# Performance work log

Hardware: AMD Instinct MI355X
Metric: run time of the kernel (lower is better)

Reference implementation:

```python
import jax, jax.numpy as jnp
import numpy as np

EPS = 1e-08


def _d_hat(d, mask, eps=EPS):
    # d: [B,N,H,W] float, mask: [B,N,H,W] bool
    B, N, H, W = mask.shape
    flat_d = d.reshape(B * N, H * W)
    flat_m = mask.reshape(B * N, H * W)
    cnt = flat_m.sum(axis=1)  # [BN] int
    # masked median: push invalid entries to +inf, sort, pick lower-median index
    sorted_v = jnp.sort(jnp.where(flat_m, flat_d, jnp.inf), axis=1)
    idx = jnp.maximum((cnt - 1) // 2, 0)
    med = jnp.take_along_axis(sorted_v, idx[:, None], axis=1)[:, 0]
    med = jnp.where(cnt > 0, med, jnp.zeros_like(med))  # empty mask -> median 0
    cnt_f = jnp.maximum(cnt, 1).astype(d.dtype)
    # masked MAD scale (mean abs deviation over valid pixels) + eps
    abs_sum = (jnp.abs(flat_d - med[:, None]) * flat_m).sum(axis=1)
    sc = jnp.where(cnt > 0, abs_sum / cnt_f + eps, jnp.full_like(abs_sum, eps))
    d_hat = (flat_d - med[:, None]) / sc[:, None]
    return d_hat.reshape(B, N, H, W)


def _avg_pool(x, k):
    # matches F.avg_pool2d(x, k, stride=k): crop to full windows, mean per kxk block
    B, N, H, W = x.shape
    Hk, Wk = H // k, W // k
    xc = x[..., : Hk * k, : Wk * k].reshape(B, N, Hk, k, Wk, k)
    return xc.mean(axis=(3, 5))


def _grad_loss(pred, target, mask):
    total = jnp.asarray(0.0, pred.dtype)
    mf = mask.astype(pred.dtype)
    for s in range(4):
        if s == 0:
            p, t, m = pred, target, mask
        else:
            k = 2 ** s
            p = _avg_pool(pred, k)
            t = _avg_pool(target, k)
            m = _avg_pool(mf, k) > 0  # .bool() of pooled float mask
        diff = p - t
        gx = jnp.abs(diff[..., :, 1:] - diff[..., :, :-1])
        gy = jnp.abs(diff[..., 1:, :] - diff[..., :-1, :])
        mx = m[..., :, 1:] & m[..., :, :-1]
        my = m[..., 1:, :] & m[..., :-1, :]
        lx = (gx * mx).sum() / jnp.maximum(mx.sum(), 1).astype(pred.dtype)
        ly = (gy * my).sum() / jnp.maximum(my.sum(), 1).astype(pred.dtype)
        total = total + lx + ly
    return total / 4


def setup_inputs() -> dict:
    key = jax.random.key(0)
    k1, k2, k3 = jax.random.split(key, 3)
    B, N, H, W = 4, 16, 518, 518
    pred = jax.random.normal(k1, (B, N, H, W), dtype=jnp.float32)
    y = jax.random.normal(k2, (B, N, H, W), dtype=jnp.float32)
    masks_squeezed = jax.random.bernoulli(k3, 0.9, (B, N, H, W))
    return {"pred": pred, "y": y, "masks_squeezed": masks_squeezed}


def reference(pred, y, masks_squeezed):
    mask = masks_squeezed.astype(bool)
    pred_hat = _d_hat(pred, mask)
    y_hat = _d_hat(y, mask)
    rho = jnp.abs(pred_hat - y_hat) * mask  # rho[~mask] = 0
    valid = jnp.maximum(mask.sum(axis=(2, 3)).astype(pred.dtype), 1.0)
    loss_ssi = (rho.sum(axis=(2, 3)) / valid).mean()
    loss_grad = _grad_loss(pred_hat, y_hat, mask)
    return loss_ssi + 0.5 * loss_grad
```

## Files before the change

### kernel.cpp

```cpp
#include <hip/hip_runtime.h>
#include <stdint.h>

typedef unsigned int u32;
typedef unsigned long long u64;
typedef unsigned char u8;

#define NIMG 64
#define W0   518
#define H0   518
#define HW   268324
#define HW4  67081
#define BPI  32
#define NB0  33
#define N1 67081
#define N2 16641
#define CAP 32768
#define LCAP 1024

#define OFF_CNT   0ULL
#define OFF_CCNT  256ULL
#define OFF_NBL   768ULL
#define OFF_RHO   1280ULL
#define OFF_STOT  1792ULL
#define OFF_SBL   2816ULL
#define OFF_GI0   3840ULL
#define OFF_GI1   5888ULL
#define OFF_GI2   7936ULL
#define OFF_GI3   9984ULL
#define ZERO_END  12032ULL
#define OFF_MED   12032ULL
#define OFF_SCI   12544ULL
#define OFF_SELW  13056ULL
#define OFF_SWF   14080ULL
#define OFF_CAND  15360ULL
#define OFF_MU8   (OFF_CAND + 16777216ULL)
#define OFF_P1    (OFF_MU8 + 17172736ULL)
#define OFF_M1    (OFF_P1 + 17172736ULL)
#define OFF_P2    (OFF_M1 + 4293184ULL)
#define OFF_M2    (OFF_P2 + 4260096ULL)

__device__ __forceinline__ u32 f2key(float f) {
  u32 u = __float_as_uint(f);
  return (u & 0x80000000u) ? ~u : (u | 0x80000000u);
}
__device__ __forceinline__ float key2f(u32 k) {
  u32 u = (k & 0x80000000u) ? (k & 0x7fffffffu) : ~k;
  return __uint_as_float(u);
}

__device__ void blk_rankfind(u32* h, u32 target, bool enable, u32* outBin, u32* outRank)
{
  int b0 = threadIdx.x * 8;
  u32 s = 0;
  for (int j = 0; j < 8; j++) s += h[b0 + j];
  u32 x = s;
  int lane = threadIdx.x & 63;
  for (int o = 1; o < 64; o <<= 1) {
    u32 v = __shfl_up(x, o, 64);
    if (lane >= o) x += v;
  }
  __shared__ u32 wsum[4];
  int wv = threadIdx.x >> 6;
  if (lane == 63) wsum[wv] = x;
  __syncthreads();
  u32 woff = 0;
  for (int w = 0; w < wv; w++) woff += wsum[w];
  u32 cum = woff + x - s;
  for (int j = 0; j < 8; j++) {
    u32 v = h[b0 + j];
    if (enable && target >= cum && target < cum + v) { *outBin = (u32)(b0 + j); *outRank = target - cum; }
    cum += v;
  }
  __syncthreads();
}

__global__ __launch_bounds__(256) void k_sample(const float* __restrict__ p,
    const float* __restrict__ y, u32* __restrict__ selw, float* __restrict__ swf,
    u32* __restrict__ zbase)
{
  int t = blockIdx.x, img = t >> 1;
  if (t == 0) {
    for (int i = threadIdx.x; i < 3008; i += 256) zbase[i] = 0;
  }
  const float* src = ((t & 1) ? y : p) + (size_t)img * HW;
  __shared__ u32 h[2048];
  __shared__ u32 bLo, rT, bHi;
  if (threadIdx.x == 0) { bLo = 0; bHi = 2047; }
  for (int i = threadIdx.x; i < 2048; i += 256) h[i] = 0;
  __syncthreads();
  for (int j = 0; j < 16; j++) {
    int s = threadIdx.x * 16 + j;
    float v = src[s * 65 + 32];
    atomicAdd(&h[f2key(v) >> 21], 1u);
  }
  __syncthreads();
  blk_rankfind(h, 1919u, true, &bLo, &rT);
  blk_rankfind(h, 2175u, true, &bHi, &rT);
  if (threadIdx.x == 0) {
    u32 k0 = bLo << 21;
    u32 k1 = (bHi >= 2047u) ? 0xFFFFFFFFu : ((bHi + 1u) << 21);
    selw[2 * t + 0] = k0;
    selw[2 * t + 1] = k1;
    float f0 = (k0 <= 0x007FFFFFu) ? __uint_as_float(0xFF800000u) : key2f(k0);
    float f1 = (k1 >= 0xFF800000u) ? __uint_as_float(0x7F800000u) : key2f(k1);
    swf[2 * t + 0] = f0;
    swf[2 * t + 1] = f1;
  }
}

__global__ __launch_bounds__(256) void k_scan0(const float4* __restrict__ p,
    const float4* __restrict__ y, const int4* __restrict__ m,
    uchar4* __restrict__ mu4, const float* __restrict__ swf,
    float* __restrict__ cand, u32* __restrict__ ccnt, u32* __restrict__ cnt,
    double* __restrict__ Stot, u32* __restrict__ Nbl, double* __restrict__ Sbl)
{
  __shared__ float capP[LCAP], capY[LCAP];
  __shared__ u32 nP, nY, baseP, baseY;
  if (threadIdx.x == 0) { nP = 0; nY = 0; }
  __syncthreads();
  int img = blockIdx.x / BPI, blk = blockIdx.x % BPI;
  float f0P = swf[img * 4 + 0], f1P = swf[img * 4 + 1];
  float f0Y = swf[img * 4 + 2], f1Y = swf[img * 4 + 3];
  const float4* pb = p + (size_t)img * HW4;
  const float4* yb = y + (size_t)img * HW4;
  const int4* mb = m + (size_t)img * HW4;
  uchar4* mo = mu4 + (size_t)img * HW4;
  int lc = 0, nBp = 0, nBy = 0;
  float sTp = 0.f, sBp = 0.f, sTy = 0.f, sBy = 0.f;

#define PEL(mm, vp, vy) if (mm) { lc++; \
      sTp += vp; \
      if (vp < f0P) { nBp++; sBp += vp; } \
      else if (vp < f1P) { u32 ix = atomicAdd(&nP, 1u); if (ix < LCAP) capP[ix] = vp; } \
      sTy += vy; \
      if (vy < f0Y) { nBy++; sBy += vy; } \
      else if (vy < f1Y) { u32 ix = atomicAdd(&nY, 1u); if (ix < LCAP) capY[ix] = vy; } }
#define PGRP(idx) { \
      float4 pv = pb[idx]; float4 yv = yb[idx]; int4 mv = mb[idx]; \
      uchar4 mw; mw.x = mv.x ? 1 : 0; mw.y = mv.y ? 1 : 0; mw.z = mv.z ? 1 : 0; mw.w = mv.w ? 1 : 0; \
      mo[idx] = mw; \
      PEL(mw.x, pv.x, yv.x) PEL(mw.y, pv.y, yv.y) PEL(mw.z, pv.z, yv.z) PEL(mw.w, pv.w, yv.w) }

  const int S = BPI * 256;
  int i = blk * 256 + threadIdx.x;
  for (; i + S < HW4; i += 2 * S) {
    float4 pa = pb[i], pc = pb[i + S];
    float4 ya = yb[i], yc = yb[i + S];
    int4 ma = mb[i], mc = mb[i + S];
    uchar4 wa, wc;
    wa.x = ma.x ? 1 : 0; wa.y = ma.y ? 1 : 0; wa.z = ma.z ? 1 : 0; wa.w = ma.w ? 1 : 0;
    wc.x = mc.x ? 1 : 0; wc.y = mc.y ? 1 : 0; wc.z = mc.z ? 1 : 0; wc.w = mc.w ? 1 : 0;
    mo[i] = wa; mo[i + S] = wc;
    PEL(wa.x, pa.x, ya.x) PEL(wa.y, pa.y, ya.y) PEL(wa.z, pa.z, ya.z) PEL(wa.w, pa.w, ya.w)
    PEL(wc.x, pc.x, yc.x) PEL(wc.y, pc.y, yc.y) PEL(wc.z, pc.z, yc.z) PEL(wc.w, pc.w, yc.w)
  }
  if (i < HW4) PGRP(i)
#undef PGRP
#undef PEL

  __syncthreads();
  if (threadIdx.x == 0) {
    u32 np = nP, ny = nY;
    u32 addP = (np > (u32)LCAP) ? (u32)(CAP + 1) : np;
    u32 addY = (ny > (u32)LCAP) ? (u32)(CAP + 1) : ny;
    baseP = atomicAdd(&ccnt[img * 2 + 0], addP);
    baseY = atomicAdd(&ccnt[img * 2 + 1], addY);
  }
  __syncthreads();
  {
    u32 np = min(nP, (u32)LCAP), ny = min(nY, (u32)LCAP);
    float* cp = cand + (size_t)(img * 2 + 0) * CAP;
    float* cy = cand + (size_t)(img * 2 + 1) * CAP;
    for (u32 k = threadIdx.x; k < np; k += 256) { u32 g = baseP + k; if (g < CAP) cp[g] = capP[k]; }
    for (u32 k = threadIdx.x; k < ny; k += 256) { u32 g = baseY + k; if (g < CAP) cy[g] = capY[k]; }
  }
  double v0 = (double)sTp, v1 = (double)sBp, v2 = (double)sTy, v3 = (double)sBy;
  double v4 = (double)lc, v5 = (double)nBp, v6 = (double)nBy;
  for (int o = 32; o; o >>= 1) {
    v0 += __shfl_down(v0, o, 64); v1 += __shfl_down(v1, o, 64);
    v2 += __shfl_down(v2, o, 64); v3 += __shfl_down(v3, o, 64);
    v4 += __shfl_down(v4, o, 64); v5 += __shfl_down(v5, o, 64);
    v6 += __shfl_down(v6, o, 64);
  }
  __shared__ double sh[7][4];
  int lane = threadIdx.x & 63, wv = threadIdx.x >> 6;
  if (lane == 0) { sh[0][wv]=v0; sh[1][wv]=v1; sh[2][wv]=v2; sh[3][wv]=v3; sh[4][wv]=v4; sh[5][wv]=v5; sh[6][wv]=v6; }
  __syncthreads();
  if (threadIdx.x == 0) {
    double a[7];
    for (int k = 0; k < 7; k++) a[k] = sh[k][0] + sh[k][1] + sh[k][2] + sh[k][3];
    atomicAdd(&Stot[img * 2 + 0], a[0]);
    atomicAdd(&Sbl [img * 2 + 0], a[1]);
    atomicAdd(&Stot[img * 2 + 1], a[2]);
    atomicAdd(&Sbl [img * 2 + 1], a[3]);
    atomicAdd(&cnt[img], (u32)a[4]);
    atomicAdd(&Nbl[img * 2 + 0], (u32)a[5]);
    atomicAdd(&Nbl[img * 2 + 1], (u32)a[6]);
  }
}

__global__ __launch_bounds__(256) void k_med2(const float* __restrict__ cand,
    const u32* __restrict__ ccnt, const u32* __restrict__ cnt,
    const u32* __restrict__ Nbl, const double* __restrict__ Stot,
    const double* __restrict__ Sbl, const u32* __restrict__ selw,
    const float* __restrict__ pf, const float* __restrict__ yf,
    const u8* __restrict__ mu8, float* __restrict__ med, float* __restrict__ sci)
{
  int t = blockIdx.x, img = t >> 1;
  u32 c = cnt[img];
  if (c == 0) {
    if (threadIdx.x == 0) { med[t] = 0.f; sci[t] = 1e8f; }
    return;
  }
  u32 ntot = ccnt[t];
  u32 target0 = (c - 1) >> 1;
  u32 nb = Nbl[t];
  bool valid = (ntot <= (u32)CAP) && (target0 >= nb) && ((target0 - nb) < ntot);
  __shared__ u32 h[2048];
  __shared__ u32 sBin, sRank;
  if (threadIdx.x == 0) { sBin = 0; sRank = 0; }
  int lane = threadIdx.x & 63, wv = threadIdx.x >> 6;
  __shared__ double sh2[2][4];

  if (valid) {
    u32 n = ntot;
    const float* cd = cand + (size_t)t * CAP;
    u32 curLo = selw[2 * t + 0];
    u64 curR = (u64)selw[2 * t + 1] - (u64)curLo;
    u32 tgt = target0 - nb;
    for (int pass = 0; pass < 3; pass++) {
      int s = 0;
      while (((curR - 1) >> s) >= 2048) s++;
      for (int i = threadIdx.x; i < 2048; i += 256) h[i] = 0;
      __syncthreads();
      for (u32 j = threadIdx.x; j < n; j += 256) {
        u32 k = f2key(cd[j]);
        if (k >= curLo && (u64)(k - curLo) < curR)
          atomicAdd(&h[(k - curLo) >> s], 1u);
      }
      __syncthreads();
      blk_rankfind(h, tgt, true, &sBin, &sRank);
      curLo = curLo + (sBin << s);
      curR = (u64)1 << s;
      tgt = sRank;
      if (s == 0) break;
    }
    float mv = key2f(curLo);
    u32 nlt2 = 0; float slt2 = 0.f;
    for (u32 j = threadIdx.x; j < n; j += 256) {
      float v = cd[j];
      if (v < mv) { nlt2++; slt2 += v; }
    }
    double v0 = (double)nlt2, v1 = (double)slt2;
    for (int o = 32; o; o >>= 1) { v0 += __shfl_down(v0, o, 64); v1 += __shfl_down(v1, o, 64); }
    if (lane == 0) { sh2[0][wv] = v0; sh2[1][wv] = v1; }
    __syncthreads();
    if (threadIdx.x == 0) {
      double nl = (double)nb + sh2[0][0] + sh2[0][1] + sh2[0][2] + sh2[0][3];
      double sl = Sbl[t] + sh2[1][0] + sh2[1][1] + sh2[1][2] + sh2[1][3];
      double md = (double)mv;
      double mad = Stot[t] + 2.0 * md * nl - 2.0 * sl - md * (double)c;
      double sc = mad / (double)c + 1e-8;
      med[t] = mv; sci[t] = (float)(1.0 / sc);
    }
  } else {
    const float* src = ((t & 1) ? yf : pf) + (size_t)img * HW;
    const u8* mk = mu8 + (size_t)img * HW;
    u32 curLo = 0; u64 curR = (u64)1 << 32; u32 tgt = target0;
    for (int pass = 0; pass < 4; pass++) {
      int s = 0;
      while (((curR - 1) >> s) >= 2048) s++;
      for (int i = threadIdx.x; i < 2048; i += 256) h[i] = 0;
      __syncthreads();
      for (u32 j = threadIdx.x; j < (u32)HW; j += 256) {
        if (mk[j]) {
          u32 k = f2key(src[j]);
          if (k >= curLo && (u64)(k - curLo) < curR)
            atomicAdd(&h[(k - curLo) >> s], 1u);
        }
      }
      __syncthreads();
      blk_rankfind(h, tgt, true, &sBin, &sRank);
      curLo = curLo + (sBin << s);
      curR = (u64)1 << s;
      tgt = sRank;
      if (s == 0) break;
    }
    float mv = key2f(curLo);
    double nl = 0.0, sl = 0.0;
    for (u32 j = threadIdx.x; j < (u32)HW; j += 256) {
      if (mk[j]) {
        float v = src[j];
        if (v < mv) { nl += 1.0; sl += (double)v; }
      }
    }
    for (int o = 32; o; o >>= 1) { nl += __shfl_down(nl, o, 64); sl += __shfl_down(sl, o, 64); }
    if (lane == 0) { sh2[0][wv] = nl; sh2[1][wv] = sl; }
    __syncthreads();
    if (threadIdx.x == 0) {
      double nlT = sh2[0][0] + sh2[0][1] + sh2[0][2] + sh2[0][3];
      double slT = sh2[1][0] + sh2[1][1] + sh2[1][2] + sh2[1][3];
      double md = (double)mv;
      double mad = Stot[t] + 2.0 * md * nlT - 2.0 * slT - md * (double)c;
      double sc = mad / (double)c + 1e-8;
      med[t] = mv; sci[t] = (float)(1.0 / sc);
    }
  }
}

__global__ __launch_bounds__(320) void k_fuse0(const float* __restrict__ p,
    const float* __restrict__ y, const u8* __restrict__ mu,
    const float* __restrict__ medv, const float* __restrict__ sciv,
    float* __restrict__ P1, u8* __restrict__ M1,
    double* __restrict__ rho, double* __restrict__ gI)
{
  int img = blockIdx.x / NB0, band = blockIdx.x % NB0;
  float mp = medv[img * 2 + 0], my = medv[img * 2 + 1];
  float ap = sciv[img * 2 + 0], ay = sciv[img * 2 + 1];
  const float* pb = p + (size_t)img * HW;
  const float* yb = y + (size_t)img * HW;
  const u8*   mb = mu + (size_t)img * HW;
  int ra = band * 16;
  int rb = min(ra + 16, H0);
  int rend = (rb < H0) ? rb + 1 : H0;
  int oc = threadIdx.x;
  bool act = oc < 259;
  int cc = act ? 2 * oc : 516;
  bool vn = act && (2 * oc + 2 < W0);
  int lane = threadIdx.x & 63;
  bool edge = (lane == 63);
  float gx = 0.f, gy = 0.f, rr = 0.f;
  int cx = 0, cy = 0;
  float pd0 = 0.f, pd1 = 0.f; u8 pm0 = 0, pm1 = 0;
  float2 pv0, yv0, pv1, yv1;
  uchar2 mv0, mv1;
  {
    size_t a0 = (size_t)ra * W0 + cc;
    pv0 = *(const float2*)(pb + a0); yv0 = *(const float2*)(yb + a0); mv0 = *(const uchar2*)(mb + a0);
    if (ra + 1 < rend) {
      size_t a1 = a0 + W0;
      pv1 = *(const float2*)(pb + a1); yv1 = *(const float2*)(yb + a1); mv1 = *(const uchar2*)(mb + a1);
    } else { pv1 = pv0; yv1 = yv0; mv1 = mv0; }
  }
  for (int r = ra; r < rend; ++r) {
    float2 pv2 = pv1, yv2 = yv1; uchar2 mv2 = mv1;
    if (r + 2 < rend) {
      size_t a2 = (size_t)(r + 2) * W0 + cc;
      pv2 = *(const float2*)(pb + a2); yv2 = *(const float2*)(yb + a2); mv2 = *(const uchar2*)(mb + a2);
    }
    bool core = r < rb;
    float d0 = (pv0.x - mp) * ap - (yv0.x - my) * ay;
    float d1 = (pv0.y - mp) * ap - (yv0.y - my) * ay;
    u8 m0 = mv0.x, m1 = mv0.y;
    float dn = __shfl_down(d0, 1, 64);
    int mn = __shfl_down((int)m0, 1, 64);
    if (vn && edge) {
      size_t a = (size_t)r * W0 + (size_t)cc + 2;
      float pnb = pb[a], ynb = yb[a];
      dn = (pnb - mp) * ap - (ynb - my) * ay;
      mn = mb[a];
    }
    if (act) {
      float f0 = (float)m0, f1 = (float)m1;
      if (core) {
        gx += f0 * f1 * fabsf(d1 - d0); cx += (int)(m0 & m1);
        if (vn) { float fn = (float)mn; gx += f1 * fn * fabsf(dn - d1); cx += (m1 && mn) ? 1 : 0; }
        rr += f0 * fabsf(d0) + f1 * fabsf(d1);
      }
      if (r > ra) {
        gy += f0 * (float)pm0 * fabsf(d0 - pd0); cy += (int)(m0 & pm0);
        gy += f1 * (float)pm1 * fabsf(d1 - pd1); cy += (int)(m1 & pm1);
      }
      if (core && (r & 1)) {
        size_t o = (size_t)img * N1 + (size_t)(r >> 1) * 259 + oc;
        P1[o] = 0.25f * (pd0 + pd1 + d0 + d1);
        M1[o] = (u8)((pm0 | pm1 | m0 | m1) ? 1 : 0);
      }
    }
    pd0 = d0; pd1 = d1; pm0 = m0; pm1 = m1;
    pv0 = pv1; yv0 = yv1; mv0 = mv1;
    pv1 = pv2; yv1 = yv2; mv1 = mv2;
  }
  double v0 = (double)gx, v1 = (double)cx, v2 = (double)gy, v3 = (double)cy, v4 = (double)rr;
  for (int o = 32; o; o >>= 1) {
    v0 += __shfl_down(v0, o, 64); v1 += __shfl_down(v1, o, 64);
    v2 += __shfl_down(v2, o, 64); v3 += __shfl_down(v3, o, 64);
    v4 += __shfl_down(v4, o, 64);
  }
  __shared__ double sh[5][5];
  int wv = threadIdx.x >> 6;
  if (lane == 0) { sh[0][wv] = v0; sh[1][wv] = v1; sh[2][wv] = v2; sh[3][wv] = v3; sh[4][wv] = v4; }
  __syncthreads();
  if (threadIdx.x == 0) {
    double a0 = 0, a1 = 0, a2 = 0, a3 = 0, a4 = 0;
    for (int w = 0; w < 5; w++) { a0 += sh[0][w]; a1 += sh[1][w]; a2 += sh[2][w]; a3 += sh[3][w]; a4 += sh[4][w]; }
    atomicAdd(&gI[img * 4 + 0], a0);
    atomicAdd(&gI[img * 4 + 1], a1);
    atomicAdd(&gI[img * 4 + 2], a2);
    atomicAdd(&gI[img * 4 + 3], a3);
    atomicAdd(&rho[img], a4);
  }
}

__global__ void k_gp(const float* __restrict__ Pin,
    const u8* __restrict__ Min, float* __restrict__ Pout, u8* __restrict__ Mout,
    int Win, int Hin, int Wout, int Hout, int nb, double* __restrict__ gI)
{
  int img = blockIdx.x / nb, band = blockIdx.x % nb;
  int npixI = Win * Hin, npixO = Wout * Hout;
  const float* pb = Pin + (size_t)img * npixI;
  const u8* mb = Min + (size_t)img * npixI;
  int poolEnd = 2 * Hout;
  int ra = band * 16;
  int rb = min(ra + 16, poolEnd);
  int rbx = (band == nb - 1) ? Hin : rb;
  int rend = (rbx < Hin) ? rbx + 1 : Hin;
  float gx = 0.f, gy = 0.f;
  int cx = 0, cy = 0;
  int oc = threadIdx.x;
  if (oc < Wout) {
    int c0 = 2 * oc, c1 = c0 + 1, cn = c0 + 2;
    bool vn = cn < Win;
    bool gyn = vn && (cn >= 2 * Wout);
    float pd0 = 0.f, pd1 = 0.f, pdn = 0.f;
    u8 pm0 = 0, pm1 = 0, pmn = 0;
    for (int r = ra; r < rend; ++r) {
      bool core = r < rbx;
      int base = r * Win;
      float d0 = pb[base + c0], d1 = pb[base + c1];
      u8 m0 = mb[base + c0], m1 = mb[base + c1];
      float dn = 0.f; u8 mn = 0;
      if (vn) { dn = pb[base + cn]; mn = mb[base + cn]; }
      if (core) {
        if (m0 & m1) { gx += fabsf(d1 - d0); cx++; }
        if (vn && (m1 & mn)) { gx += fabsf(dn - d1); cx++; }
      }
      if (r > ra) {
        if (m0 & pm0) { gy += fabsf(d0 - pd0); cy++; }
        if (m1 & pm1) { gy += fabsf(d1 - pd1); cy++; }
        if (gyn && (mn & pmn)) { gy += fabsf(dn - pdn); cy++; }
      }
      if (core && (r & 1) && r < poolEnd) {
        size_t o = (size_t)img * npixO + (size_t)(r >> 1) * Wout + oc;
        Pout[o] = 0.25f * (pd0 + pd1 + d0 + d1);
        Mout[o] = (u8)((pm0 | pm1 | m0 | m1) ? 1 : 0);
      }
      pd0 = d0; pd1 = d1; pdn = dn; pm0 = m0; pm1 = m1; pmn = mn;
    }
  }
  double v0 = (double)gx, v1 = (double)cx, v2 = (double)gy, v3 = (double)cy;
  for (int o = 32; o; o >>= 1) {
    v0 += __shfl_down(v0, o, 64); v1 += __shfl_down(v1, o, 64);
    v2 += __shfl_down(v2, o, 64); v3 += __shfl_down(v3, o, 64);
  }
  __shared__ double sh[4][4];
  int lane = threadIdx.x & 63, wv = threadIdx.x >> 6;
  int nw = (blockDim.x + 63) >> 6;
  if (lane == 0) { sh[0][wv] = v0; sh[1][wv] = v1; sh[2][wv] = v2; sh[3][wv] = v3; }
  __syncthreads();
  if (threadIdx.x == 0) {
    double a0 = 0, a1 = 0, a2 = 0, a3 = 0;
    for (int w = 0; w < nw; w++) { a0 += sh[0][w]; a1 += sh[1][w]; a2 += sh[2][w]; a3 += sh[3][w]; }
    atomicAdd(&gI[img * 4 + 0], a0);
    atomicAdd(&gI[img * 4 + 1], a1);
    atomicAdd(&gI[img * 4 + 2], a2);
    atomicAdd(&gI[img * 4 + 3], a3);
  }
}

__global__ __launch_bounds__(64) void k_gp_last(const float* __restrict__ Pin,
    const u8* __restrict__ Min, double* __restrict__ gI2v, double* __restrict__ gI3v)
{
  const int Win = 129, Hin = 129, Wout = 64, nb = 8;
  int img = blockIdx.x / nb, band = blockIdx.x % nb;
  const float* pb = Pin + (size_t)img * (Win * Hin);
  const u8* mb = Min + (size_t)img * (Win * Hin);
  int ra = band * 16;
  int rb = min(ra + 16, 128);
  int rbx = (band == nb - 1) ? Hin : rb;
  int rend2 = (band < nb - 1) ? (ra + 18) : Hin;
  float gx = 0.f, gy = 0.f; int cx = 0, cy = 0;
  float ogx = 0.f, ogy = 0.f; int ocx = 0, ocy = 0;
  int oc = threadIdx.x;
  int c0 = 2 * oc, c1 = c0 + 1, cn = c0 + 2;
  bool vn = cn < Win;
  bool gyn = vn && (cn >= 2 * Wout);
  float pd0 = 0.f, pd1 = 0.f, pdn = 0.f;
  u8 pm0 = 0, pm1 = 0, pmn = 0;
  float ppo = 0.f; int pmo = 0; bool havePrev = false;
  for (int r = ra; r < rend2; ++r) {
    int base = r * Win;
    float d0 = pb[base + c0], d1 = pb[base + c1];
    u8 m0 = mb[base + c0], m1 = mb[base + c1];
    float dn = 0.f; u8 mn = 0;
    if (vn) { dn = pb[base + cn]; mn = mb[base + cn]; }
    if (r < rbx) {
      if (m0 & m1) { gx += fabsf(d1 - d0); cx++; }
      if (vn && (m1 & mn)) { gx += fabsf(dn - d1); cx++; }
    }
    if (r > ra && r <= rb) {
      if (m0 & pm0) { gy += fabsf(d0 - pd0); cy++; }
      if (m1 & pm1) { gy += fabsf(d1 - pd1); cy++; }
      if (gyn && (mn & pmn)) { gy += fabsf(dn - pdn); cy++; }
    }
    if (r & 1) {
      bool owned = r < rb;
      bool halo = (r == rb + 1);
      if (owned || halo) {
        float po = 0.25f * (pd0 + pd1 + d0 + d1);
        int mo = (pm0 | pm1 | m0 | m1) ? 1 : 0;
        float pon = __shfl_down(po, 1, 64);
        int mon = __shfl_down(mo, 1, 64);
        if (owned && oc < 63 && mo && mon) { ogx += fabsf(pon - po); ocx++; }
        if (havePrev && mo && pmo) { ogy += fabsf(po - ppo); ocy++; }
        ppo = po; pmo = mo; havePrev = true;
      }
    }
    pd0 = d0; pd1 = d1; pdn = dn; pm0 = m0; pm1 = m1; pmn = mn;
  }
  double v[8] = {(double)gx, (double)cx, (double)gy, (double)cy,
                 (double)ogx, (double)ocx, (double)ogy, (double)ocy};
  for (int o = 32; o; o >>= 1)
    for (int k = 0; k < 8; k++) v[k] += __shfl_down(v[k], o, 64);
  if (threadIdx.x == 0) {
    atomicAdd(&gI2v[img * 4 + 0], v[0]);
    atomicAdd(&gI2v[img * 4 + 1], v[1]);
    atomicAdd(&gI2v[img * 4 + 2], v[2]);
    atomicAdd(&gI2v[img * 4 + 3], v[3]);
    atomicAdd(&gI3v[img * 4 + 0], v[4]);
    atomicAdd(&gI3v[img * 4 + 1], v[5]);
    atomicAdd(&gI3v[img * 4 + 2], v[6]);
    atomicAdd(&gI3v[img * 4 + 3], v[7]);
  }
}

__global__ void k_final(const double* __restrict__ rho, const u32* __restrict__ cnt,
    const double* __restrict__ gI0, const double* __restrict__ gI1,
    const double* __restrict__ gI2, const double* __restrict__ gI3,
    float* __restrict__ out)
{
  int i = threadIdx.x;
  double v[17];
  double c = cnt[i] ? (double)cnt[i] : 1.0;
  v[0] = rho[i] / c;
  for (int j = 0; j < 4; j++) {
    v[1 + 0 * 4 + j] = gI0[i * 4 + j];
    v[1 + 1 * 4 + j] = gI1[i * 4 + j];
    v[1 + 2 * 4 + j] = gI2[i * 4 + j];
    v[1 + 3 * 4 + j] = gI3[i * 4 + j];
  }
  for (int o = 32; o; o >>= 1)
    for (int k = 0; k < 17; k++) v[k] += __shfl_down(v[k], o, 64);
  if (i == 0) {
    double ssi = v[0] / (double)NIMG;
    double g = 0.0;
    for (int s = 0; s < 4; s++) {
      double gxs = v[1 + s * 4 + 0], cxs = v[1 + s * 4 + 1];
      double gys = v[1 + s * 4 + 2], cys = v[1 + s * 4 + 3];
      g += gxs / (cxs > 1.0 ? cxs : 1.0);
      g += gys / (cys > 1.0 ? cys : 1.0);
    }
    g /= 4.0;
    out[0] = (float)(ssi + 0.5 * g);
  }
}

extern "C" void kernel_launch(void* const* d_in, const int* in_sizes, int n_in,
                              void* d_out, int out_size, void* d_ws, size_t ws_size,
                              hipStream_t stream) {
  (void)in_sizes; (void)n_in; (void)out_size; (void)ws_size;
  const float4* p4 = (const float4*)d_in[0];
  const float4* y4 = (const float4*)d_in[1];
  const int4* m4 = (const int4*)d_in[2];
  const float* pf = (const float*)d_in[0];
  const float* yf = (const float*)d_in[1];
  u8* ws = (u8*)d_ws;

  u32*    cnt  = (u32*)(ws + OFF_CNT);
  u32*    ccnt = (u32*)(ws + OFF_CCNT);
  u32*    Nbl  = (u32*)(ws + OFF_NBL);
  double* rho  = (double*)(ws + OFF_RHO);
  double* Stot = (double*)(ws + OFF_STOT);
  double* Sbl  = (double*)(ws + OFF_SBL);
  double* gI0  = (double*)(ws + OFF_GI0);
  double* gI1  = (double*)(ws + OFF_GI1);
  double* gI2  = (double*)(ws + OFF_GI2);
  double* gI3  = (double*)(ws + OFF_GI3);
  float*  med  = (float*)(ws + OFF_MED);
  float*  sci  = (float*)(ws + OFF_SCI);
  u32*    selw = (u32*)(ws + OFF_SELW);
  float*  swf  = (float*)(ws + OFF_SWF);
  float*  cand = (float*)(ws + OFF_CAND);
  u8*     mu8  = (u8*)(ws + OFF_MU8);
  float*  P1   = (float*)(ws + OFF_P1);
  u8*     M1   = (u8*)(ws + OFF_M1);
  float*  P2   = (float*)(ws + OFF_P2);
  u8*     M2   = (u8*)(ws + OFF_M2);

  k_sample<<<128, 256, 0, stream>>>(pf, yf, selw, swf, (u32*)ws);
  k_scan0<<<NIMG * BPI, 256, 0, stream>>>(p4, y4, m4, (uchar4*)mu8, swf, cand, ccnt, cnt, Stot, Nbl, Sbl);
  k_med2<<<128, 256, 0, stream>>>(cand, ccnt, cnt, Nbl, Stot, Sbl, selw, pf, yf, mu8, med, sci);
  k_fuse0<<<NIMG * NB0, 320, 0, stream>>>(pf, yf, mu8, med, sci, P1, M1, rho, gI0);
  k_gp<<<NIMG * 17, 192, 0, stream>>>(P1, M1, P2, M2, 259, 259, 129, 129, 17, gI1);
  k_gp_last<<<NIMG * 8, 64, 0, stream>>>(P2, M2, gI2, gI3);
  k_final<<<1, 64, 0, stream>>>(rho, cnt, gI0, gI1, gI2, gI3, (float*)d_out);
}
```

Measured before the change: 366.1 us.

## Fuse pyramid levels 1-3 and final reduction into one kernel with ticket

Merges the level-1 gradient/pool kernel, the level-2/3 kernel and the final reduction kernel into a single kernel. Level-2 pooled rows are held in a shared-memory double buffer and level-3 values are computed from them, so the P2/M2 intermediates are no longer written to or read from global memory. A last-block ticket counter performs the final reduction. This removes two launches and a global round trip, at the cost of per-row __syncthreads and some halo recomputation.

```diff
diff --git a/kernel.cpp b/kernel.cpp
--- a/kernel.cpp
+++ b/kernel.cpp
@@ -13,7 +13,6 @@
 #define BPI  32
 #define NB0  33
 #define N1 67081
-#define N2 16641
 #define CAP 32768
 #define LCAP 1024
 
@@ -27,17 +26,16 @@
 #define OFF_GI1   5888ULL
 #define OFF_GI2   7936ULL
 #define OFF_GI3   9984ULL
-#define ZERO_END  12032ULL
-#define OFF_MED   12032ULL
-#define OFF_SCI   12544ULL
-#define OFF_SELW  13056ULL
-#define OFF_SWF   14080ULL
+#define OFF_TKT   12032ULL
+#define ZERO_END  12288ULL
+#define OFF_MED   12288ULL
+#define OFF_SCI   12800ULL
+#define OFF_SELW  13312ULL
+#define OFF_SWF   14336ULL
 #define OFF_CAND  15360ULL
 #define OFF_MU8   (OFF_CAND + 16777216ULL)
 #define OFF_P1    (OFF_MU8 + 17172736ULL)
 #define OFF_M1    (OFF_P1 + 17172736ULL)
-#define OFF_P2    (OFF_M1 + 4293184ULL)
-#define OFF_M2    (OFF_P2 + 4260096ULL)
 
 __device__ __forceinline__ u32 f2key(float f) {
   u32 u = __float_as_uint(f);
@@ -80,7 +78,7 @@
 {
   int t = blockIdx.x, img = t >> 1;
   if (t == 0) {
-    for (int i = threadIdx.x; i < 3008; i += 256) zbase[i] = 0;
+    for (int i = threadIdx.x; i < 3072; i += 256) zbase[i] = 0;
   }
   const float* src = ((t & 1) ? y : p) + (size_t)img * HW;
   __shared__ u32 h[2048];
@@ -135,11 +133,6 @@
       sTy += vy; \
       if (vy < f0Y) { nBy++; sBy += vy; } \
       else if (vy < f1Y) { u32 ix = atomicAdd(&nY, 1u); if (ix < LCAP) capY[ix] = vy; } }
-#define PGRP(idx) { \
-      float4 pv = pb[idx]; float4 yv = yb[idx]; int4 mv = mb[idx]; \
-      uchar4 mw; mw.x = mv.x ? 1 : 0; mw.y = mv.y ? 1 : 0; mw.z = mv.z ? 1 : 0; mw.w = mv.w ? 1 : 0; \
-      mo[idx] = mw; \
-      PEL(mw.x, pv.x, yv.x) PEL(mw.y, pv.y, yv.y) PEL(mw.z, pv.z, yv.z) PEL(mw.w, pv.w, yv.w) }
 
   const int S = BPI * 256;
   int i = blk * 256 + threadIdx.x;
@@ -154,8 +147,12 @@
     PEL(wa.x, pa.x, ya.x) PEL(wa.y, pa.y, ya.y) PEL(wa.z, pa.z, ya.z) PEL(wa.w, pa.w, ya.w)
     PEL(wc.x, pc.x, yc.x) PEL(wc.y, pc.y, yc.y) PEL(wc.z, pc.z, yc.z) PEL(wc.w, pc.w, yc.w)
   }
-  if (i < HW4) PGRP(i)
-#undef PGRP
+  if (i < HW4) {
+    float4 pv = pb[i]; float4 yv = yb[i]; int4 mv = mb[i];
+    uchar4 mw; mw.x = mv.x ? 1 : 0; mw.y = mv.y ? 1 : 0; mw.z = mv.z ? 1 : 0; mw.w = mv.w ? 1 : 0;
+    mo[i] = mw;
+    PEL(mw.x, pv.x, yv.x) PEL(mw.y, pv.y, yv.y) PEL(mw.z, pv.z, yv.z) PEL(mw.w, pv.w, yv.w)
+  }
 #undef PEL
 
   __syncthreads();
@@ -402,166 +399,154 @@
   }
 }
 
-__global__ void k_gp(const float* __restrict__ Pin,
-    const u8* __restrict__ Min, float* __restrict__ Pout, u8* __restrict__ Mout,
-    int Win, int Hin, int Wout, int Hout, int nb, double* __restrict__ gI)
+__global__ __launch_bounds__(192) void k_gp12(const float* __restrict__ P1,
+    const u8* __restrict__ M1, const double* __restrict__ rho,
+    const u32* __restrict__ cnt, const double* __restrict__ gI0,
+    double* __restrict__ gI1v, double* __restrict__ gI2v, double* __restrict__ gI3v,
+    u32* __restrict__ ticket, float* __restrict__ out)
 {
+  const int Win = 259, Hin = 259;
+  const int nb = 17;
   int img = blockIdx.x / nb, band = blockIdx.x % nb;
-  int npixI = Win * Hin, npixO = Wout * Hout;
-  const float* pb = Pin + (size_t)img * npixI;
-  const u8* mb = Min + (size_t)img * npixI;
-  int poolEnd = 2 * Hout;
+  const float* pb = P1 + (size_t)img * (Win * Hin);
+  const u8*   mb = M1 + (size_t)img * (Win * Hin);
   int ra = band * 16;
-  int rb = min(ra + 16, poolEnd);
+  int rb = min(ra + 16, 258);
   int rbx = (band == nb - 1) ? Hin : rb;
-  int rend = (rbx < Hin) ? rbx + 1 : Hin;
-  float gx = 0.f, gy = 0.f;
-  int cx = 0, cy = 0;
+  int rendCore = (rbx < Hin) ? rbx + 1 : Hin;
+  int rend = min(ra + 20, Hin);
+  if (rend < rendCore) rend = rendCore;
+  int p2own0 = ra >> 1, p2own1 = rb >> 1;
+  int p3own0 = 4 * band, p3own1 = min(4 * band + 4, 64);
+
+  __shared__ float l2v[2][132];
+  __shared__ u8    l2m[2][132];
+
   int oc = threadIdx.x;
-  if (oc < Wout) {
-    int c0 = 2 * oc, c1 = c0 + 1, cn = c0 + 2;
-    bool vn = cn < Win;
-    bool gyn = vn && (cn >= 2 * Wout);
-    float pd0 = 0.f, pd1 = 0.f, pdn = 0.f;
-    u8 pm0 = 0, pm1 = 0, pmn = 0;
-    for (int r = ra; r < rend; ++r) {
-      bool core = r < rbx;
-      int base = r * Win;
-      float d0 = pb[base + c0], d1 = pb[base + c1];
-      u8 m0 = mb[base + c0], m1 = mb[base + c1];
-      float dn = 0.f; u8 mn = 0;
-      if (vn) { dn = pb[base + cn]; mn = mb[base + cn]; }
-      if (core) {
-        if (m0 & m1) { gx += fabsf(d1 - d0); cx++; }
-        if (vn && (m1 & mn)) { gx += fabsf(dn - d1); cx++; }
-      }
-      if (r > ra) {
-        if (m0 & pm0) { gy += fabsf(d0 - pd0); cy++; }
-        if (m1 & pm1) { gy += fabsf(d1 - pd1); cy++; }
-        if (gyn && (mn & pmn)) { gy += fabsf(dn - pdn); cy++; }
-      }
-      if (core && (r & 1) && r < poolEnd) {
-        size_t o = (size_t)img * npixO + (size_t)(r >> 1) * Wout + oc;
-        Pout[o] = 0.25f * (pd0 + pd1 + d0 + d1);
-        Mout[o] = (u8)((pm0 | pm1 | m0 | m1) ? 1 : 0);
-      }
-      pd0 = d0; pd1 = d1; pdn = dn; pm0 = m0; pm1 = m1; pmn = mn;
-    }
-  }
-  double v0 = (double)gx, v1 = (double)cx, v2 = (double)gy, v3 = (double)cy;
-  for (int o = 32; o; o >>= 1) {
-    v0 += __shfl_down(v0, o, 64); v1 += __shfl_down(v1, o, 64);
-    v2 += __shfl_down(v2, o, 64); v3 += __shfl_down(v3, o, 64);
-  }
-  __shared__ double sh[4][4];
+  bool act = oc < 129;
+  int c0 = act ? 2 * oc : 256;
+  int c1 = c0 + 1, cnn = c0 + 2;
+  bool vn = act && (cnn < Win);
+  bool gyn = vn && (cnn >= 258);
+
+  float g1x = 0, g1y = 0, g2x = 0, g2y = 0, g3x = 0, g3y = 0;
+  int   c1x = 0, c1y = 0, c2x = 0, c2y = 0, c3x = 0, c3y = 0;
+
+  float pd0 = 0, pd1 = 0, pdn = 0; u8 pm0 = 0, pm1 = 0, pmn = 0;
+  float p2prev = 0; int m2prev = 0; bool have2 = false;
+  float p3prev = 0; int m3prev = 0; bool have3 = false;
+
+  for (int r = ra; r < rend; ++r) {
+    int base = r * Win;
+    float d0 = 0, d1 = 0, dn = 0; u8 m0 = 0, m1 = 0, mn = 0;
+    if (act) {
+      d0 = pb[base + c0]; d1 = pb[base + c1];
+      m0 = mb[base + c0]; m1 = mb[base + c1];
+      if (vn) { dn = pb[base + cnn]; mn = mb[base + cnn]; }
+    }
+    if (act && r < rbx) {
+      if (m0 & m1) { g1x += fabsf(d1 - d0); c1x++; }
+      if (vn && (m1 & mn)) { g1x += fabsf(dn - d1); c1x++; }
+    }
+    if (act && r > ra && r < rendCore) {
+      if (m0 & pm0) { g1y += fabsf(d0 - pd0); c1y++; }
+      if (m1 & pm1) { g1y += fabsf(d1 - pd1); c1y++; }
+      if (gyn && (mn & pmn)) { g1y += fabsf(dn - pdn); c1y++; }
+    }
+    if (r & 1) {
+      int j2 = r >> 1;
+      if (j2 < 129) {
+        int buf = j2 & 1;
+        float v2 = 0; u8 mm2 = 0;
+        if (act) {
+          v2 = 0.25f * (pd0 + pd1 + d0 + d1);
+          mm2 = (u8)((pm0 | pm1 | m0 | m1) ? 1 : 0);
+          l2v[buf][oc] = v2; l2m[buf][oc] = mm2;
+        }
+        __syncthreads();
+        if (act && j2 >= p2own0 && j2 < p2own1 && oc < 128) {
+          float vr = l2v[buf][oc + 1]; u8 mr = l2m[buf][oc + 1];
+          if (mm2 & mr) { g2x += fabsf(vr - v2); c2x++; }
+        }
+        if (act && have2 && (j2 - 1) >= p2own0 && (j2 - 1) < p2own1) {
+          if (mm2 && m2prev) { g2y += fabsf(v2 - p2prev); c2y++; }
+        }
+        if ((j2 & 1) && threadIdx.x < 64) {
+          int i3 = j2 >> 1;
+          int pbuf = buf ^ 1;
+          int tc = 2 * threadIdx.x;
+          float a = l2v[pbuf][tc], b = l2v[pbuf][tc + 1];
+          float cf = l2v[buf][tc], df = l2v[buf][tc + 1];
+          u8 ma_ = l2m[pbuf][tc], mb_ = l2m[pbuf][tc + 1];
+          u8 mc_ = l2m[buf][tc],  md_ = l2m[buf][tc + 1];
+          float v3 = 0.25f * (a + b + cf + df);
+          int m3i = (ma_ | mb_ | mc_ | md_) ? 1 : 0;
+          float vn3 = __shfl_down(v3, 1, 64);
+          int   mn3 = __shfl_down(m3i, 1, 64);
+          if (i3 >= p3own0 && i3 < p3own1) {
+            if (threadIdx.x < 63 && m3i && mn3) { g3x += fabsf(vn3 - v3); c3x++; }
+          }
+          if (have3 && (i3 - 1) >= p3own0 && (i3 - 1) < p3own1) {
+            if (m3i && m3prev) { g3y += fabsf(v3 - p3prev); c3y++; }
+          }
+          p3prev = v3; m3prev = m3i; have3 = true;
+        }
+        __syncthreads();
+        if (act) { p2prev = v2; m2prev = mm2; have2 = true; }
+      }
+    }
+    pd0 = d0; pd1 = d1; pdn = dn; pm0 = m0; pm1 = m1; pmn = mn;
+  }
+
+  double v[12] = {(double)g1x, (double)c1x, (double)g1y, (double)c1y,
+                  (double)g2x, (double)c2x, (double)g2y, (double)c2y,
+                  (double)g3x, (double)c3x, (double)g3y, (double)c3y};
+  for (int o = 32; o; o >>= 1)
+    for (int k = 0; k < 12; k++) v[k] += __shfl_down(v[k], o, 64);
+  __shared__ double shr[12][3];
   int lane = threadIdx.x & 63, wv = threadIdx.x >> 6;
-  int nw = (blockDim.x + 63) >> 6;
-  if (lane == 0) { sh[0][wv] = v0; sh[1][wv] = v1; sh[2][wv] = v2; sh[3][wv] = v3; }
+  if (lane == 0) for (int k = 0; k < 12; k++) shr[k][wv] = v[k];
   __syncthreads();
   if (threadIdx.x == 0) {
-    double a0 = 0, a1 = 0, a2 = 0, a3 = 0;
-    for (int w = 0; w < nw; w++) { a0 += sh[0][w]; a1 += sh[1][w]; a2 += sh[2][w]; a3 += sh[3][w]; }
-    atomicAdd(&gI[img * 4 + 0], a0);
-    atomicAdd(&gI[img * 4 + 1], a1);
-    atomicAdd(&gI[img * 4 + 2], a2);
-    atomicAdd(&gI[img * 4 + 3], a3);
-  }
-}
-
-__global__ __launch_bounds__(64) void k_gp_last(const float* __restrict__ Pin,
-    const u8* __restrict__ Min, double* __restrict__ gI2v, double* __restrict__ gI3v)
-{
-  const int Win = 129, Hin = 129, Wout = 64, nb = 8;
-  int img = blockIdx.x / nb, band = blockIdx.x % nb;
-  const float* pb = Pin + (size_t)img * (Win * Hin);
-  const u8* mb = Min + (size_t)img * (Win * Hin);
-  int ra = band * 16;
-  int rb = min(ra + 16, 128);
-  int rbx = (band == nb - 1) ? Hin : rb;
-  int rend2 = (band < nb - 1) ? (ra + 18) : Hin;
-  float gx = 0.f, gy = 0.f; int cx = 0, cy = 0;
-  float ogx = 0.f, ogy = 0.f; int ocx = 0, ocy = 0;
-  int oc = threadIdx.x;
-  int c0 = 2 * oc, c1 = c0 + 1, cn = c0 + 2;
-  bool vn = cn < Win;
-  bool gyn = vn && (cn >= 2 * Wout);
-  float pd0 = 0.f, pd1 = 0.f, pdn = 0.f;
-  u8 pm0 = 0, pm1 = 0, pmn = 0;
-  float ppo = 0.f; int pmo = 0; bool havePrev = false;
-  for (int r = ra; r < rend2; ++r) {
-    int base = r * Win;
-    float d0 = pb[base + c0], d1 = pb[base + c1];
-    u8 m0 = mb[base + c0], m1 = mb[base + c1];
-    float dn = 0.f; u8 mn = 0;
-    if (vn) { dn = pb[base + cn]; mn = mb[base + cn]; }
-    if (r < rbx) {
-      if (m0 & m1) { gx += fabsf(d1 - d0); cx++; }
-      if (vn && (m1 & mn)) { gx += fabsf(dn - d1); cx++; }
-    }
-    if (r > ra && r <= rb) {
-      if (m0 & pm0) { gy += fabsf(d0 - pd0); cy++; }
-      if (m1 & pm1) { gy += fabsf(d1 - pd1); cy++; }
-      if (gyn && (mn & pmn)) { gy += fabsf(dn - pdn); cy++; }
-    }
-    if (r & 1) {
-      bool owned = r < rb;
-      bool halo = (r == rb + 1);
-      if (owned || halo) {
-        float po = 0.25f * (pd0 + pd1 + d0 + d1);
-        int mo = (pm0 | pm1 | m0 | m1) ? 1 : 0;
-        float pon = __shfl_down(po, 1, 64);
-        int mon = __shfl_down(mo, 1, 64);
-        if (owned && oc < 63 && mo && mon) { ogx += fabsf(pon - po); ocx++; }
-        if (havePrev && mo && pmo) { ogy += fabsf(po - ppo); ocy++; }
-        ppo = po; pmo = mo; havePrev = true;
-      }
-    }
-    pd0 = d0; pd1 = d1; pdn = dn; pm0 = m0; pm1 = m1; pmn = mn;
-  }
-  double v[8] = {(double)gx, (double)cx, (double)gy, (double)cy,
-                 (double)ogx, (double)ocx, (double)ogy, (double)ocy};
-  for (int o = 32; o; o >>= 1)
-    for (int k = 0; k < 8; k++) v[k] += __shfl_down(v[k], o, 64);
+    for (int k = 0; k < 4; k++) {
+      atomicAdd(&gI1v[img * 4 + k], shr[k][0] + shr[k][1] + shr[k][2]);
+      atomicAdd(&gI2v[img * 4 + k], shr[4 + k][0] + shr[4 + k][1] + shr[4 + k][2]);
+      atomicAdd(&gI3v[img * 4 + k], shr[8 + k][0] + shr[8 + k][1] + shr[8 + k][2]);
+    }
+  }
+  __threadfence();
+  __shared__ u32 isLast;
   if (threadIdx.x == 0) {
-    atomicAdd(&gI2v[img * 4 + 0], v[0]);
-    atomicAdd(&gI2v[img * 4 + 1], v[1]);
-    atomicAdd(&gI2v[img * 4 + 2], v[2]);
-    atomicAdd(&gI2v[img * 4 + 3], v[3]);
-    atomicAdd(&gI3v[img * 4 + 0], v[4]);
-    atomicAdd(&gI3v[img * 4 + 1], v[5]);
-    atomicAdd(&gI3v[img * 4 + 2], v[6]);
-    atomicAdd(&gI3v[img * 4 + 3], v[7]);
-  }
-}
-
-__global__ void k_final(const double* __restrict__ rho, const u32* __restrict__ cnt,
-    const double* __restrict__ gI0, const double* __restrict__ gI1,
-    const double* __restrict__ gI2, const double* __restrict__ gI3,
-    float* __restrict__ out)
-{
-  int i = threadIdx.x;
-  double v[17];
-  double c = cnt[i] ? (double)cnt[i] : 1.0;
-  v[0] = rho[i] / c;
-  for (int j = 0; j < 4; j++) {
-    v[1 + 0 * 4 + j] = gI0[i * 4 + j];
-    v[1 + 1 * 4 + j] = gI1[i * 4 + j];
-    v[1 + 2 * 4 + j] = gI2[i * 4 + j];
-    v[1 + 3 * 4 + j] = gI3[i * 4 + j];
-  }
-  for (int o = 32; o; o >>= 1)
-    for (int k = 0; k < 17; k++) v[k] += __shfl_down(v[k], o, 64);
-  if (i == 0) {
-    double ssi = v[0] / (double)NIMG;
-    double g = 0.0;
-    for (int s = 0; s < 4; s++) {
-      double gxs = v[1 + s * 4 + 0], cxs = v[1 + s * 4 + 1];
-      double gys = v[1 + s * 4 + 2], cys = v[1 + s * 4 + 3];
-      g += gxs / (cxs > 1.0 ? cxs : 1.0);
-      g += gys / (cys > 1.0 ? cys : 1.0);
-    }
-    g /= 4.0;
-    out[0] = (float)(ssi + 0.5 * g);
+    u32 old = atomicAdd(ticket, 1u);
+    isLast = (old == (u32)(gridDim.x - 1)) ? 1u : 0u;
+  }
+  __syncthreads();
+  if (isLast && threadIdx.x < 64) {
+    __threadfence();
+    int i = threadIdx.x;
+    double vv[17];
+    double c = cnt[i] ? (double)cnt[i] : 1.0;
+    vv[0] = rho[i] / c;
+    for (int j = 0; j < 4; j++) {
+      vv[1 + j]  = gI0[i * 4 + j];
+      vv[5 + j]  = atomicAdd(&gI1v[i * 4 + j], 0.0);
+      vv[9 + j]  = atomicAdd(&gI2v[i * 4 + j], 0.0);
+      vv[13 + j] = atomicAdd(&gI3v[i * 4 + j], 0.0);
+    }
+    for (int o = 32; o; o >>= 1)
+      for (int k = 0; k < 17; k++) vv[k] += __shfl_down(vv[k], o, 64);
+    if (i == 0) {
+      double ssi = vv[0] / (double)NIMG;
+      double g = 0.0;
+      for (int s = 0; s < 4; s++) {
+        double gxs = vv[1 + s * 4 + 0], cxs = vv[1 + s * 4 + 1];
+        double gys = vv[1 + s * 4 + 2], cys = vv[1 + s * 4 + 3];
+        g += gxs / (cxs > 1.0 ? cxs : 1.0);
+        g += gys / (cys > 1.0 ? cys : 1.0);
+      }
+      g /= 4.0;
+      out[0] = (float)(ssi + 0.5 * g);
+    }
   }
 }
 
@@ -586,6 +571,7 @@
   double* gI1  = (double*)(ws + OFF_GI1);
   double* gI2  = (double*)(ws + OFF_GI2);
   double* gI3  = (double*)(ws + OFF_GI3);
+  u32*    tkt  = (u32*)(ws + OFF_TKT);
   float*  med  = (float*)(ws + OFF_MED);
   float*  sci  = (float*)(ws + OFF_SCI);
   u32*    selw = (u32*)(ws + OFF_SELW);
@@ -594,14 +580,10 @@
   u8*     mu8  = (u8*)(ws + OFF_MU8);
   float*  P1   = (float*)(ws + OFF_P1);
   u8*     M1   = (u8*)(ws + OFF_M1);
-  float*  P2   = (float*)(ws + OFF_P2);
-  u8*     M2   = (u8*)(ws + OFF_M2);
 
   k_sample<<<128, 256, 0, stream>>>(pf, yf, selw, swf, (u32*)ws);
   k_scan0<<<NIMG * BPI, 256, 0, stream>>>(p4, y4, m4, (uchar4*)mu8, swf, cand, ccnt, cnt, Stot, Nbl, Sbl);
   k_med2<<<128, 256, 0, stream>>>(cand, ccnt, cnt, Nbl, Stot, Sbl, selw, pf, yf, mu8, med, sci);
   k_fuse0<<<NIMG * NB0, 320, 0, stream>>>(pf, yf, mu8, med, sci, P1, M1, rho, gI0);
-  k_gp<<<NIMG * 17, 192, 0, stream>>>(P1, M1, P2, M2, 259, 259, 129, 129, 17, gI1);
-  k_gp_last<<<NIMG * 8, 64, 0, stream>>>(P2, M2, gI2, gI3);
-  k_final<<<1, 64, 0, stream>>>(rho, cnt, gI0, gI1, gI2, gI3, (float*)d_out);
-}
+  k_gp12<<<NIMG * 17, 192, 0, stream>>>(P1, M1, rho, cnt, gI0, gI1, gI2, gI3, tkt, (float*)d_out);
+}
```

Result: slower. 421.6 us (+15.2%).
